# Kernel optimization log

Measured on AMD Instinct MI355X. Metric: run time of the kernel, lower is better.

The kernel has to match this reference:

```python
import jax, jax.numpy as jnp
import numpy as np

B, H, W0, C0 = 64, 50, 500, 3
TOPK = 10
OUT_SHAPE = (50, 3)


def _p(key, shape, scale=0.02):
    return (jax.random.normal(key, shape, dtype=jnp.float32) * scale)


def setup_inputs() -> dict:
    key = jax.random.key(0)
    ks = jax.random.split(key, 20)
    flat_dim = 128 * H * (W0 // 100) + TOPK * (32 + 64 + 128) * H  # 144000
    return {
        "x": jax.random.normal(ks[0], (B, H, W0, C0), dtype=jnp.float32),
        "c1w1": _p(ks[1], (C0, 32)), "c1b1": jnp.zeros((32,), jnp.float32),
        "c1w2": _p(ks[2], (32, 32)), "c1b2": jnp.zeros((32,), jnp.float32),
        "a1W": _p(ks[3], (H, 32)), "a1b": jnp.zeros((H, W0), jnp.float32),
        "c2w1": _p(ks[4], (32, 64)), "c2b1": jnp.zeros((64,), jnp.float32),
        "c2w2": _p(ks[5], (64, 64)), "c2b2": jnp.zeros((64,), jnp.float32),
        "a2W": _p(ks[6], (H, 64)), "a2b": jnp.zeros((H, W0 // 5), jnp.float32),
        "c3w1": _p(ks[7], (64, 128)), "c3b1": jnp.zeros((128,), jnp.float32),
        "c3w2": _p(ks[8], (128, 128)), "c3b2": jnp.zeros((128,), jnp.float32),
        "a3W": _p(ks[9], (H, 128)), "a3b": jnp.zeros((H, W0 // 25), jnp.float32),
        "fc1w": _p(ks[10], (flat_dim, 1024)), "fc1b": jnp.zeros((1024,), jnp.float32),
        "fc2w": _p(ks[11], (1024, 1024)), "fc2b": jnp.zeros((1024,), jnp.float32),
        "fc3w": _p(ks[12], (1024, OUT_SHAPE[0] * OUT_SHAPE[1])),
        "fc3b": jnp.zeros((OUT_SHAPE[0] * OUT_SHAPE[1],), jnp.float32),
    }


def _conv1x1_relu(x, w, b):
    # x: (B,H,W,Cin) channels-last; 1x1 conv == per-pixel matmul
    return jax.nn.relu(jnp.einsum('bhwc,co->bhwo', x, w) + b)


def _att_topk(x, Wm, bm, k):
    # x: (B,H,W,C); Wm: (H,C); bm: (H,W). Batched over all H rows at once.
    e = jnp.tanh(jnp.einsum('bhwc,hc->bhw', x, Wm) + bm[None])
    _, idx = jax.lax.top_k(e, k)                       # (B,H,k), sorted desc
    feats = jnp.take_along_axis(x, idx[..., None], axis=2)  # (B,H,k,C)
    return feats.reshape(x.shape[0], -1)  # row-major (h,k,c) matches torch cat


def _maxpool_w(x, p):
    b, h, w, c = x.shape
    return x.reshape(b, h, w // p, p, c).max(axis=3)


def reference(x, c1w1, c1b1, c1w2, c1b2, a1W, a1b, c2w1, c2b1, c2w2, c2b2,
              a2W, a2b, c3w1, c3b1, c3w2, c3b2, a3W, a3b,
              fc1w, fc1b, fc2w, fc2b, fc3w, fc3b):
    b = x.shape[0]
    x1 = _conv1x1_relu(_conv1x1_relu(x, c1w1, c1b1), c1w2, c1b2)   # (B,H,500,32)
    xa1 = _att_topk(x1, a1W, a1b, TOPK)
    x2 = _maxpool_w(x1, 5)                                          # (B,H,100,32)
    x2 = _conv1x1_relu(_conv1x1_relu(x2, c2w1, c2b1), c2w2, c2b2)   # (B,H,100,64)
    xa2 = _att_topk(x2, a2W, a2b, TOPK)
    x3 = _maxpool_w(x2, 5)                                          # (B,H,20,64)
    x3 = _conv1x1_relu(_conv1x1_relu(x3, c3w1, c3b1), c3w2, c3b2)   # (B,H,20,128)
    xa3 = _att_topk(x3, a3W, a3b, TOPK)
    xp = _maxpool_w(x3, 4)                                          # (B,H,5,128)
    # torch flattens NCHW: transpose to (B,C,H,W) before flatten
    xf = jnp.transpose(xp, (0, 3, 1, 2)).reshape(b, -1)
    z = jnp.concatenate([xa1, xa2, xa3, xf], axis=1)                # (B,144000)
    z = jax.nn.relu(z @ fc1w + fc1b)
    z = z @ fc2w + fc2b  # fc2 has no activation in the original
    # dropout is identity at inference
    z = z @ fc3w + fc3b
    return z.reshape(b, *OUT_SHAPE)
```

## Files before the change

kernel.cpp:

```cpp
#include <hip/hip_runtime.h>
#include <math.h>

#define DEV __device__ __forceinline__
DEV float frelu(float x) { return x > 0.f ? x : 0.f; }

typedef float f4 __attribute__((ext_vector_type(4)));
typedef short bf16x8 __attribute__((ext_vector_type(8)));
typedef int   i2x  __attribute__((ext_vector_type(2)));

DEV unsigned pack_hi2(float a, float b) {
    return (__float_as_uint(b) & 0xFFFF0000u) | (__float_as_uint(a) >> 16);
}
DEV float hi_part(float a) {
    return __uint_as_float(__float_as_uint(a) & 0xFFFF0000u);
}

#define DPP_ADD(v, ctrl) \
    ((v) + __int_as_float(__builtin_amdgcn_update_dpp(0, __float_as_int(v), (ctrl), 0xf, 0xf, true)))

DEV float rdlane(float v, int l) {
    return __int_as_float(__builtin_amdgcn_readlane(__float_as_int(v), l));
}

#define NG1 8
__global__ __launch_bounds__(256) void k_s1(
    const float* __restrict__ x,
    const float* __restrict__ w1, const float* __restrict__ b1,
    const float* __restrict__ w2, const float* __restrict__ b2,
    const float* __restrict__ aW, const float* __restrict__ ab,
    float* __restrict__ x1p, float* __restrict__ e1)
{
    __shared__ float v1s[4][2][32];
    int tid = threadIdx.x;
    int wv = tid >> 6, lane = tid & 63;
    int half = lane >> 5, o = lane & 31;
    int hs = blockIdx.x * 8 + wv * 2 + half;

    float W1c0 = w1[o], W1c1 = w1[32 + o], W1c2 = w1[64 + o], B1 = b1[o];
    float W2[32];
#pragma unroll
    for (int i = 0; i < 32; ++i) W2[i] = w2[i * 32 + o];
    float B2 = b2[o];
    float* vs = &v1s[wv][half][0];

#pragma unroll 1
    for (int i = 0; i < NG1; ++i) {
        int g = hs * NG1 + i;
        int b = g / 5000, r = g % 5000, h = r / 100, pw = r % 100;
        float AWo = aW[h * 32 + o];
        const float* xrow = x + (size_t)((b * 50 + h) * 500) * 3;
        float vmax = 0.f;
#pragma unroll 1
        for (int j = 0; j < 5; ++j) {
            int w = pw * 5 + j;
            float x0 = xrow[w * 3 + 0], x1v = xrow[w * 3 + 1], x2v = xrow[w * 3 + 2];
            float v1 = frelu(fmaf(x0, W1c0, fmaf(x1v, W1c1, fmaf(x2v, W1c2, B1))));
            vs[o] = v1;
            float a2 = B2;
#pragma unroll
            for (int q = 0; q < 32; q += 4) {
                float4 v4 = *(const float4*)&vs[q];
                a2 = fmaf(v4.x, W2[q + 0], a2);
                a2 = fmaf(v4.y, W2[q + 1], a2);
                a2 = fmaf(v4.z, W2[q + 2], a2);
                a2 = fmaf(v4.w, W2[q + 3], a2);
            }
            float t = frelu(a2);
            vmax = fmaxf(vmax, t);
            float ep = t * AWo;
            ep = DPP_ADD(ep, 0x111);
            ep = DPP_ADD(ep, 0x112);
            ep = DPP_ADD(ep, 0x114);
            ep = DPP_ADD(ep, 0x118);
            ep = DPP_ADD(ep, 0x142);
            if (o == 31) e1[(b * 50 + h) * 500 + w] = ep + ab[h * 500 + w];
        }
        x1p[(size_t)g * 32 + o] = vmax;
    }
}

#define NG2 16
__global__ __launch_bounds__(256) void k_s2(
    const float* __restrict__ x1p,
    const float* __restrict__ w1, const float* __restrict__ b1,
    const float* __restrict__ w2, const float* __restrict__ b2,
    const float* __restrict__ aW, const float* __restrict__ ab,
    float* __restrict__ x2p, float* __restrict__ e2)
{
    __shared__ float v1s[4][64];
    int tid = threadIdx.x;
    int wv = tid >> 6, o = tid & 63;
    int slot = blockIdx.x * 4 + wv;

    float W1[32];
#pragma unroll
    for (int i = 0; i < 32; ++i) W1[i] = w1[i * 64 + o];
    float W2[64];
#pragma unroll
    for (int i = 0; i < 64; ++i) W2[i] = w2[i * 64 + o];
    float B1 = b1[o], B2 = b2[o];
    float* vs = &v1s[wv][0];

#pragma unroll 1
    for (int i = 0; i < NG2; ++i) {
        int g = slot * NG2 + i;
        int b = g / 1000, r = g % 1000, h = r / 20, pw = r % 20;
        float AWo = aW[h * 64 + o];
        float vmax = 0.f;
#pragma unroll 1
        for (int j = 0; j < 5; ++j) {
            int w = pw * 5 + j;
            const float* in = x1p + (size_t)((b * 50 + h) * 100 + w) * 32;
            float a1 = B1;
#pragma unroll
            for (int q = 0; q < 32; q += 4) {
                float4 a4 = *(const float4*)&in[q];
                a1 = fmaf(a4.x, W1[q + 0], a1);
                a1 = fmaf(a4.y, W1[q + 1], a1);
                a1 = fmaf(a4.z, W1[q + 2], a1);
                a1 = fmaf(a4.w, W1[q + 3], a1);
            }
            vs[o] = frelu(a1);
            float a2 = B2;
#pragma unroll
            for (int q = 0; q < 64; q += 4) {
                float4 v4 = *(const float4*)&vs[q];
                a2 = fmaf(v4.x, W2[q + 0], a2);
                a2 = fmaf(v4.y, W2[q + 1], a2);
                a2 = fmaf(v4.z, W2[q + 2], a2);
                a2 = fmaf(v4.w, W2[q + 3], a2);
            }
            float t = frelu(a2);
            vmax = fmaxf(vmax, t);
            float ep = t * AWo;
            ep = DPP_ADD(ep, 0x111);
            ep = DPP_ADD(ep, 0x112);
            ep = DPP_ADD(ep, 0x114);
            ep = DPP_ADD(ep, 0x118);
            ep = DPP_ADD(ep, 0x142);
            ep = DPP_ADD(ep, 0x143);
            if (o == 63) e2[(b * 50 + h) * 100 + w] = ep + ab[h * 100 + w];
        }
        x2p[(size_t)g * 64 + o] = vmax;
    }
}

#define NG3 8
__global__ __launch_bounds__(256) void k_s3(
    const float* __restrict__ x2p,
    const float* __restrict__ w1, const float* __restrict__ b1,
    const float* __restrict__ w2, const float* __restrict__ b2,
    const float* __restrict__ aW, const float* __restrict__ ab,
    float* __restrict__ x3p, float* __restrict__ e3)
{
    __shared__ float v1s[2][128];
    __shared__ float epart[2][2];
    int tid = threadIdx.x;
    int wv = tid >> 6, lane = tid & 63;
    int slot = wv >> 1, oh = wv & 1;
    int o = oh * 64 + lane;
    int gs = blockIdx.x * 2 + slot;

    float W1[64];
#pragma unroll
    for (int i = 0; i < 64; ++i) W1[i] = w1[i * 128 + o];
    float W2[128];
#pragma unroll
    for (int i = 0; i < 128; ++i) W2[i] = w2[i * 128 + o];
    float B1 = b1[o], B2 = b2[o];

#pragma unroll 1
    for (int i = 0; i < NG3; ++i) {
        int g = gs * NG3 + i;
        int b = g / 250, r = g % 250, h = r / 5, pw = r % 5;
        float AWo = aW[h * 128 + o];
        float vmax = 0.f;
#pragma unroll 1
        for (int j = 0; j < 4; ++j) {
            int w = pw * 4 + j;
            const float* in = x2p + (size_t)((b * 50 + h) * 20 + w) * 64;
            float a1a = B1, a1b = 0.f;
#pragma unroll
            for (int q = 0; q < 64; q += 8) {
                float4 a4 = *(const float4*)&in[q];
                float4 b4 = *(const float4*)&in[q + 4];
                a1a = fmaf(a4.x, W1[q + 0], a1a);
                a1b = fmaf(a4.y, W1[q + 1], a1b);
                a1a = fmaf(a4.z, W1[q + 2], a1a);
                a1b = fmaf(a4.w, W1[q + 3], a1b);
                a1a = fmaf(b4.x, W1[q + 4], a1a);
                a1b = fmaf(b4.y, W1[q + 5], a1b);
                a1a = fmaf(b4.z, W1[q + 6], a1a);
                a1b = fmaf(b4.w, W1[q + 7], a1b);
            }
            v1s[slot][o] = frelu(a1a + a1b);
            __syncthreads();
            float a2a = B2, a2b = 0.f, a2c = 0.f, a2d = 0.f;
#pragma unroll
            for (int q = 0; q < 128; q += 8) {
                float4 a4 = *(const float4*)&v1s[slot][q];
                float4 b4 = *(const float4*)&v1s[slot][q + 4];
                a2a = fmaf(a4.x, W2[q + 0], a2a);
                a2b = fmaf(a4.y, W2[q + 1], a2b);
                a2c = fmaf(a4.z, W2[q + 2], a2c);
                a2d = fmaf(a4.w, W2[q + 3], a2d);
                a2a = fmaf(b4.x, W2[q + 4], a2a);
                a2b = fmaf(b4.y, W2[q + 5], a2b);
                a2c = fmaf(b4.z, W2[q + 6], a2c);
                a2d = fmaf(b4.w, W2[q + 7], a2d);
            }
            float t = frelu((a2a + a2b) + (a2c + a2d));
            vmax = fmaxf(vmax, t);
            float ep = t * AWo;
            ep = DPP_ADD(ep, 0x111);
            ep = DPP_ADD(ep, 0x112);
            ep = DPP_ADD(ep, 0x114);
            ep = DPP_ADD(ep, 0x118);
            ep = DPP_ADD(ep, 0x142);
            ep = DPP_ADD(ep, 0x143);
            if (lane == 63) epart[slot][oh] = ep;
            __syncthreads();
            if (lane == 63 && oh == 0)
                e3[(b * 50 + h) * 20 + w] = epart[slot][0] + epart[slot][1] + ab[h * 20 + w];
        }
        x3p[(size_t)g * 128 + o] = vmax;
    }
}

__global__ __launch_bounds__(64) void k_t1(
    const float* __restrict__ e1, const float* __restrict__ x,
    const float* __restrict__ w1, const float* __restrict__ b1,
    const float* __restrict__ w2, const float* __restrict__ b2,
    float* __restrict__ z)
{
    int blk = blockIdx.x; int b = blk / 50; int h = blk % 50;
    int lane = threadIdx.x;
    const float* er = e1 + (b * 50 + h) * 500;
    float ev0 = er[lane];
    float ev1 = er[64 + lane];
    float ev2 = er[128 + lane];
    float ev3 = er[192 + lane];
    float ev4 = er[256 + lane];
    float ev5 = er[320 + lane];
    float ev6 = er[384 + lane];
    float ev7 = (448 + lane < 500) ? er[448 + lane] : -1e30f;

    for (int k = 0; k < 10; ++k) {
        float bv = ev0; int bi = lane;
        if (ev1 > bv) { bv = ev1; bi = 64 + lane; }
        if (ev2 > bv) { bv = ev2; bi = 128 + lane; }
        if (ev3 > bv) { bv = ev3; bi = 192 + lane; }
        if (ev4 > bv) { bv = ev4; bi = 256 + lane; }
        if (ev5 > bv) { bv = ev5; bi = 320 + lane; }
        if (ev6 > bv) { bv = ev6; bi = 384 + lane; }
        if (ev7 > bv) { bv = ev7; bi = 448 + lane; }
#pragma unroll
        for (int d = 1; d < 64; d <<= 1) {
            float ov = __shfl_xor(bv, d, 64); int oi = __shfl_xor(bi, d, 64);
            if (ov > bv || (ov == bv && oi < bi)) { bv = ov; bi = oi; }
        }
        bool me = (bi & 63) == lane; int cs = bi >> 6;
        if (me && cs == 0) ev0 = -1e30f;
        if (me && cs == 1) ev1 = -1e30f;
        if (me && cs == 2) ev2 = -1e30f;
        if (me && cs == 3) ev3 = -1e30f;
        if (me && cs == 4) ev4 = -1e30f;
        if (me && cs == 5) ev5 = -1e30f;
        if (me && cs == 6) ev6 = -1e30f;
        if (me && cs == 7) ev7 = -1e30f;

        const float* px = x + (size_t)((b * 50 + h) * 500 + bi) * 3;
        float x0 = px[0], x1v = px[1], x2v = px[2];
        int o = lane & 31;
        float v1 = frelu(fmaf(x0, w1[o], fmaf(x1v, w1[32 + o], fmaf(x2v, w1[64 + o], b1[o]))));
        float v2 = b2[o];
#pragma unroll 8
        for (int i = 0; i < 32; ++i) v2 = fmaf(rdlane(v1, i), w2[i * 32 + o], v2);
        if (lane < 32) z[(size_t)b * 112000 + h * 320 + k * 32 + o] = frelu(v2);
    }
}

__global__ __launch_bounds__(64) void k_t2(
    const float* __restrict__ e2, const float* __restrict__ x1p,
    const float* __restrict__ w1, const float* __restrict__ b1,
    const float* __restrict__ w2, const float* __restrict__ b2,
    float* __restrict__ z)
{
    int blk = blockIdx.x; int b = blk / 50; int h = blk % 50;
    int lane = threadIdx.x;
    const float* er = e2 + (b * 50 + h) * 100;
    float ev0 = er[lane];
    float ev1 = (64 + lane < 100) ? er[64 + lane] : -1e30f;

    for (int k = 0; k < 10; ++k) {
        float bv = ev0; int bi = lane;
        if (ev1 > bv) { bv = ev1; bi = 64 + lane; }
#pragma unroll
        for (int d = 1; d < 64; d <<= 1) {
            float ov = __shfl_xor(bv, d, 64); int oi = __shfl_xor(bi, d, 64);
            if (ov > bv || (ov == bv && oi < bi)) { bv = ov; bi = oi; }
        }
        bool me = (bi & 63) == lane; int cs = bi >> 6;
        if (me && cs == 0) ev0 = -1e30f;
        if (me && cs == 1) ev1 = -1e30f;

        const float* in = x1p + (size_t)((b * 50 + h) * 100 + bi) * 32;
        float v1p0 = b1[lane], v1p1 = 0.f;
#pragma unroll 8
        for (int i = 0; i < 32; i += 2) {
            v1p0 = fmaf(in[i], w1[i * 64 + lane], v1p0);
            v1p1 = fmaf(in[i + 1], w1[(i + 1) * 64 + lane], v1p1);
        }
        float v1 = frelu(v1p0 + v1p1);
        float v2p0 = b2[lane], v2p1 = 0.f;
#pragma unroll 8
        for (int i = 0; i < 64; i += 2) {
            v2p0 = fmaf(rdlane(v1, i), w2[i * 64 + lane], v2p0);
            v2p1 = fmaf(rdlane(v1, i + 1), w2[(i + 1) * 64 + lane], v2p1);
        }
        z[(size_t)b * 112000 + 16000 + h * 640 + k * 64 + lane] = frelu(v2p0 + v2p1);
    }
}

__global__ __launch_bounds__(64) void k_t3(
    const float* __restrict__ e3, const float* __restrict__ x2p,
    const float* __restrict__ w1, const float* __restrict__ b1,
    const float* __restrict__ w2, const float* __restrict__ b2,
    float* __restrict__ z)
{
    int blk = blockIdx.x; int b = blk / 50; int h = blk % 50;
    int lane = threadIdx.x;
    const float* er = e3 + (b * 50 + h) * 20;
    float ev0 = (lane < 20) ? er[lane] : -1e30f;

    for (int k = 0; k < 10; ++k) {
        float bv = ev0; int bi = lane;
#pragma unroll
        for (int d = 1; d < 64; d <<= 1) {
            float ov = __shfl_xor(bv, d, 64); int oi = __shfl_xor(bi, d, 64);
            if (ov > bv || (ov == bv && oi < bi)) { bv = ov; bi = oi; }
        }
        if (bi == lane) ev0 = -1e30f;
        const float* in = x2p + (size_t)((b * 50 + h) * 20 + bi) * 64;
        float v1a0 = b1[lane], v1a1 = 0.f, v1b0 = b1[lane + 64], v1b1 = 0.f;
#pragma unroll 8
        for (int i = 0; i < 64; i += 2) {
            float a0 = in[i], a1 = in[i + 1];
            v1a0 = fmaf(a0, w1[i * 128 + lane], v1a0);
            v1b0 = fmaf(a0, w1[i * 128 + lane + 64], v1b0);
            v1a1 = fmaf(a1, w1[(i + 1) * 128 + lane], v1a1);
            v1b1 = fmaf(a1, w1[(i + 1) * 128 + lane + 64], v1b1);
        }
        float v1a = frelu(v1a0 + v1a1), v1b = frelu(v1b0 + v1b1);
        float v2a0 = b2[lane], v2a1 = 0.f, v2b0 = b2[lane + 64], v2b1 = 0.f;
#pragma unroll 8
        for (int i = 0; i < 64; i += 2) {
            float s0 = rdlane(v1a, i), s1 = rdlane(v1a, i + 1);
            v2a0 = fmaf(s0, w2[i * 128 + lane], v2a0);
            v2b0 = fmaf(s0, w2[i * 128 + lane + 64], v2b0);
            v2a1 = fmaf(s1, w2[(i + 1) * 128 + lane], v2a1);
            v2b1 = fmaf(s1, w2[(i + 1) * 128 + lane + 64], v2b1);
        }
#pragma unroll 8
        for (int i = 0; i < 64; i += 2) {
            float s0 = rdlane(v1b, i), s1 = rdlane(v1b, i + 1);
            v2a0 = fmaf(s0, w2[(i + 64) * 128 + lane], v2a0);
            v2b0 = fmaf(s0, w2[(i + 64) * 128 + lane + 64], v2b0);
            v2a1 = fmaf(s1, w2[(i + 65) * 128 + lane], v2a1);
            v2b1 = fmaf(s1, w2[(i + 65) * 128 + lane + 64], v2b1);
        }
        size_t base = (size_t)b * 112000 + 48000 + h * 1280 + k * 128;
        z[base + lane] = frelu(v2a0 + v2a1);
        z[base + lane + 64] = frelu(v2b0 + v2b1);
    }
}

__global__ __launch_bounds__(256) void k_zt(const float* __restrict__ z, float* __restrict__ zT)
{
    __shared__ float t[64][65];
    int f0 = blockIdx.x * 64;
    int tid = threadIdx.x;
    int fl = tid & 63, q = tid >> 6;
#pragma unroll
    for (int rr = 0; rr < 16; ++rr) {
        int m = q * 16 + rr;
        t[m][fl] = z[(size_t)m * 112000 + f0 + fl];
    }
    __syncthreads();
    int m2 = tid & 63;
#pragma unroll
    for (int rr = 0; rr < 16; ++rr) {
        int fl2 = q * 16 + rr;
        zT[(size_t)(f0 + fl2) * 64 + m2] = t[m2][fl2];
    }
}

__global__ __launch_bounds__(256) void k_xf(const float* __restrict__ x3p, float* __restrict__ zT)
{
    __shared__ float t[64][129];
    int blk = blockIdx.x;
    int h = blk / 5, pw = blk % 5;
    int tid = threadIdx.x;
    for (int idx = tid; idx < 64 * 128; idx += 256) {
        int m = idx >> 7, c = idx & 127;
        t[m][c] = x3p[(size_t)((m * 50 + h) * 5 + pw) * 128 + c];
    }
    __syncthreads();
    for (int idx = tid; idx < 64 * 128; idx += 256) {
        int c = idx >> 6, m = idx & 63;
        zT[(size_t)(112000 + c * 250 + h * 5 + pw) * 64 + m] = t[m][c];
    }
}

__global__ __launch_bounds__(256, 3) void k_gemm1(
    const float* __restrict__ AT, const float* __restrict__ W,
    float* __restrict__ part)
{
    __shared__ char smem[24576];
    const int t = threadIdx.x;
    const int lane = t & 63;
    const int wv = t >> 6;
    const int n0 = blockIdx.x << 7;
    const int kc = blockIdx.y;

    const int nw = t & 127, kqi = t >> 7;
    const int ma = t & 63,  kqa = t >> 6;

    int wadrW[4];
#pragma unroll
    for (int q = 0; q < 4; ++q)
        wadrW[q] = nw * 64 + (((kqi * 2 + (q >> 1)) ^ (nw & 3)) << 4) + ((q & 1) << 3);
    int wadrA[2];
#pragma unroll
    for (int q = 0; q < 2; ++q)
        wadrA[q] = 16384 + ma * 64 + ((kqa ^ (ma & 3)) << 4) + (q << 3);

    const int c = lane & 15, hi = lane >> 4;
    int rW[2], rA[4];
#pragma unroll
    for (int i = 0; i < 2; ++i) {
        int nl = (2 * wv + i) * 16 + c;
        rW[i] = nl * 64 + ((hi ^ (c & 3)) << 4);
    }
#pragma unroll
    for (int mf = 0; mf < 4; ++mf) {
        int ml = mf * 16 + c;
        rA[mf] = 16384 + ml * 64 + ((hi ^ (c & 3)) << 4);
    }

    f4 acc[2][4];
#pragma unroll
    for (int i = 0; i < 2; ++i)
#pragma unroll
        for (int mf = 0; mf < 4; ++mf) acc[i][mf] = (f4)0.f;

    const float* Wp = W + ((size_t)kc * 1152 + kqi * 16) * 1024 + (n0 + nw);
    const float* Ap = AT + ((size_t)kc * 1152 + kqa * 8) * 64 + ma;

    float gw[16], ga[8];
#pragma unroll
    for (int j = 0; j < 16; ++j) gw[j] = Wp[(size_t)j * 1024];
#pragma unroll
    for (int j = 0; j < 8; ++j) ga[j] = Ap[j * 64];
    Wp += 32768; Ap += 2048;

#pragma unroll 1
    for (int cc = 0; cc < 36; ++cc) {
        i2x whv[4], wlv[4], ahv[2], alv[2];
#pragma unroll
        for (int q = 0; q < 4; ++q) {
            float x0 = gw[q * 4 + 0], x1 = gw[q * 4 + 1];
            float x2 = gw[q * 4 + 2], x3 = gw[q * 4 + 3];
            whv[q].x = pack_hi2(x0, x1); whv[q].y = pack_hi2(x2, x3);
            float l0 = x0 - hi_part(x0), l1 = x1 - hi_part(x1);
            float l2 = x2 - hi_part(x2), l3 = x3 - hi_part(x3);
            wlv[q].x = pack_hi2(l0, l1); wlv[q].y = pack_hi2(l2, l3);
        }
#pragma unroll
        for (int q = 0; q < 2; ++q) {
            float x0 = ga[q * 4 + 0], x1 = ga[q * 4 + 1];
            float x2 = ga[q * 4 + 2], x3 = ga[q * 4 + 3];
            ahv[q].x = pack_hi2(x0, x1); ahv[q].y = pack_hi2(x2, x3);
            float l0 = x0 - hi_part(x0), l1 = x1 - hi_part(x1);
            float l2 = x2 - hi_part(x2), l3 = x3 - hi_part(x3);
            alv[q].x = pack_hi2(l0, l1); alv[q].y = pack_hi2(l2, l3);
        }
        __syncthreads();
#pragma unroll
        for (int q = 0; q < 4; ++q) {
            *(i2x*)(smem + wadrW[q]) = whv[q];
            *(i2x*)(smem + wadrW[q] + 8192) = wlv[q];
        }
#pragma unroll
        for (int q = 0; q < 2; ++q) {
            *(i2x*)(smem + wadrA[q]) = ahv[q];
            *(i2x*)(smem + wadrA[q] + 4096) = alv[q];
        }
        if (cc < 35) {
#pragma unroll
            for (int j = 0; j < 16; ++j) gw[j] = Wp[(size_t)j * 1024];
#pragma unroll
            for (int j = 0; j < 8; ++j) ga[j] = Ap[j * 64];
            Wp += 32768; Ap += 2048;
        }
        __syncthreads();

        bf16x8 fwh[2], fwl[2], fah[4], fal[4];
#pragma unroll
        for (int i = 0; i < 2; ++i) {
            fwh[i] = *(const bf16x8*)(smem + rW[i]);
            fwl[i] = *(const bf16x8*)(smem + rW[i] + 8192);
        }
#pragma unroll
        for (int mf = 0; mf < 4; ++mf) {
            fah[mf] = *(const bf16x8*)(smem + rA[mf]);
            fal[mf] = *(const bf16x8*)(smem + rA[mf] + 4096);
        }
#pragma unroll
        for (int i = 0; i < 2; ++i)
#pragma unroll
            for (int mf = 0; mf < 4; ++mf) {
                acc[i][mf] = __builtin_amdgcn_mfma_f32_16x16x32_bf16(fwh[i], fah[mf], acc[i][mf], 0, 0, 0);
                acc[i][mf] = __builtin_amdgcn_mfma_f32_16x16x32_bf16(fwh[i], fal[mf], acc[i][mf], 0, 0, 0);
                acc[i][mf] = __builtin_amdgcn_mfma_f32_16x16x32_bf16(fwl[i], fah[mf], acc[i][mf], 0, 0, 0);
            }
    }

    float* pb = part + ((size_t)kc * 1024 + n0) * 64;
#pragma unroll
    for (int i = 0; i < 2; ++i) {
        int nf = 2 * wv + i;
#pragma unroll
        for (int mf = 0; mf < 4; ++mf) {
#pragma unroll
            for (int q = 0; q < 4; ++q) {
                int n = nf * 16 + hi * 4 + q;
                int m = mf * 16 + c;
                pb[(size_t)n * 64 + m] = acc[i][mf][q];
            }
        }
    }
}

__global__ __launch_bounds__(256) void k_gemm(
    const float* __restrict__ AT, const float* __restrict__ W,
    float* __restrict__ part, int K, int N, int KC)
{
    int n = blockIdx.x * 256 + threadIdx.x;
    int kc = blockIdx.y;
    int k0 = kc * KC;
    int k1 = k0 + KC; if (k1 > K) k1 = K;
    float acc[64];
#pragma unroll
    for (int m = 0; m < 64; ++m) acc[m] = 0.f;
#pragma unroll 2
    for (int k = k0; k < k1; ++k) {
        float wv = W[(size_t)k * N + n];
        const float4* Ak4 = (const float4*)(AT + (size_t)k * 64);
#pragma unroll
        for (int mq = 0; mq < 16; ++mq) {
            float4 a = Ak4[mq];
            acc[4 * mq + 0] = fmaf(a.x, wv, acc[4 * mq + 0]);
            acc[4 * mq + 1] = fmaf(a.y, wv, acc[4 * mq + 1]);
            acc[4 * mq + 2] = fmaf(a.z, wv, acc[4 * mq + 2]);
            acc[4 * mq + 3] = fmaf(a.w, wv, acc[4 * mq + 3]);
        }
    }
    float4* p4 = (float4*)(part + ((size_t)kc * N + n) * 64);
#pragma unroll
    for (int mq = 0; mq < 16; ++mq)
        p4[mq] = make_float4(acc[4 * mq], acc[4 * mq + 1], acc[4 * mq + 2], acc[4 * mq + 3]);
}

__global__ __launch_bounds__(256) void k_redA(
    const float* __restrict__ part, float* __restrict__ pp)
{
    int id = blockIdx.x * 256 + threadIdx.x;
    int r = id & 16383; int s = id >> 14;
    const f4* p = (const f4*)part;
    f4 v = (f4)0.f;
#pragma unroll 5
    for (int cidx = s * 25; cidx < s * 25 + 25; ++cidx)
        v += p[(size_t)cidx * 16384 + r];
    ((f4*)pp)[(size_t)s * 16384 + r] = v;
}

__global__ __launch_bounds__(256) void k_redB(
    const float* __restrict__ pp, const float* __restrict__ bias,
    float* __restrict__ h1T)
{
    int id = blockIdx.x * 256 + threadIdx.x;
    int mq = id & 15, n = id >> 4;
    const f4* p = (const f4*)pp;
    f4 s = (f4)0.f;
#pragma unroll
    for (int cidx = 0; cidx < 5; ++cidx) s += p[(size_t)cidx * 16384 + id];
    float bv = bias[n];
    s += bv;
    s.x = frelu(s.x); s.y = frelu(s.y); s.z = frelu(s.z); s.w = frelu(s.w);
    *(f4*)(h1T + (size_t)n * 64 + mq * 4) = s;
}

__global__ __launch_bounds__(256) void k_red(
    const float* __restrict__ part, const float* __restrict__ bias,
    float* __restrict__ outM, int N, int C)
{
    int id = blockIdx.x * 256 + threadIdx.x;
    int mq = id & 15, n = id >> 4;
    f4 s = (f4)0.f;
    for (int cidx = 0; cidx < C; ++cidx)
        s += *(const f4*)(part + ((size_t)cidx * N + n) * 64 + mq * 4);
    float bv = bias[n];
    s += bv;
    outM[(size_t)(mq * 4 + 0) * N + n] = s.x;
    outM[(size_t)(mq * 4 + 1) * N + n] = s.y;
    outM[(size_t)(mq * 4 + 2) * N + n] = s.z;
    outM[(size_t)(mq * 4 + 3) * N + n] = s.w;
}

__global__ __launch_bounds__(192) void k_fc3(
    const float* __restrict__ h2M, const float* __restrict__ w3,
    const float* __restrict__ b3, float* __restrict__ out)
{
    int m = blockIdx.x;
    int o = threadIdx.x;
    int oc = o < 150 ? o : 149;
    const float* hr = h2M + (size_t)m * 1024;
    float s = b3[oc];
#pragma unroll 8
    for (int k = 0; k < 1024; ++k) s = fmaf(hr[k], w3[k * 150 + oc], s);
    if (o < 150) out[m * 150 + o] = s;
}

extern "C" void kernel_launch(void* const* d_in, const int* in_sizes, int n_in,
                              void* d_out, int out_size, void* d_ws, size_t ws_size,
                              hipStream_t stream) {
    const float* X    = (const float*)d_in[0];
    const float* c1w1 = (const float*)d_in[1];
    const float* c1b1 = (const float*)d_in[2];
    const float* c1w2 = (const float*)d_in[3];
    const float* c1b2 = (const float*)d_in[4];
    const float* a1W  = (const float*)d_in[5];
    const float* a1b  = (const float*)d_in[6];
    const float* c2w1 = (const float*)d_in[7];
    const float* c2b1 = (const float*)d_in[8];
    const float* c2w2 = (const float*)d_in[9];
    const float* c2b2 = (const float*)d_in[10];
    const float* a2W  = (const float*)d_in[11];
    const float* a2b  = (const float*)d_in[12];
    const float* c3w1 = (const float*)d_in[13];
    const float* c3b1 = (const float*)d_in[14];
    const float* c3w2 = (const float*)d_in[15];
    const float* c3b2 = (const float*)d_in[16];
    const float* a3W  = (const float*)d_in[17];
    const float* a3b  = (const float*)d_in[18];
    const float* fc1w = (const float*)d_in[19];
    const float* fc1b = (const float*)d_in[20];
    const float* fc2w = (const float*)d_in[21];
    const float* fc2b = (const float*)d_in[22];
    const float* fc3w = (const float*)d_in[23];
    const float* fc3b = (const float*)d_in[24];

    float* ws  = (float*)d_ws;
    float* x1p = ws;
    float* x2p = ws + 10240000;
    float* x3p = ws + 14336000;
    float* e1  = ws + 16384000;
    float* e2  = ws + 17984000;
    float* e3  = ws + 18304000;
    float* z   = ws + 18368000;
    float* zT  = ws + 25536000;
    float* p1  = ws;
    float* pp  = ws + 16384000;
    float* h1T = ws + 16600000;
    float* p2  = ws + 16700000;
    float* h2M = ws + 21000000;

    k_s1<<<5000, 256, 0, stream>>>(X, c1w1, c1b1, c1w2, c1b2, a1W, a1b, x1p, e1);
    k_t1<<<3200, 64, 0, stream>>>(e1, X, c1w1, c1b1, c1w2, c1b2, z);
    k_s2<<<1000, 256, 0, stream>>>(x1p, c2w1, c2b1, c2w2, c2b2, a2W, a2b, x2p, e2);
    k_t2<<<3200, 64, 0, stream>>>(e2, x1p, c2w1, c2b1, c2w2, c2b2, z);
    k_s3<<<1000, 256, 0, stream>>>(x2p, c3w1, c3b1, c3w2, c3b2, a3W, a3b, x3p, e3);
    k_t3<<<3200, 64, 0, stream>>>(e3, x2p, c3w1, c3b1, c3w2, c3b2, z);
    k_zt<<<1750, 256, 0, stream>>>(z, zT);
    k_xf<<<250, 256, 0, stream>>>(x3p, zT);

    k_gemm1<<<dim3(8, 125), 256, 0, stream>>>(zT, fc1w, p1);
    k_redA<<<320, 256, 0, stream>>>(p1, pp);
    k_redB<<<64, 256, 0, stream>>>(pp, fc1b, h1T);
    k_gemm<<<dim3(4, 64), 256, 0, stream>>>(h1T, fc2w, p2, 1024, 1024, 16);
    k_red<<<64, 256, 0, stream>>>(p2, fc2b, h2M, 1024, 64);
    k_fc3<<<64, 192, 0, stream>>>(h2M, fc3w, fc3b, (float*)d_out);
}
```

Measured before the change: 883.2 us.

## Replace LDS broadcast in conv second layers with DPP row-rotate cross-lane matvec

The second 1x1 conv layer in stages 1-3 used to write each lane's activation to shared memory and read it back as broadcast float4s. It now rotates values within 16-lane rows using DPP row_ror, plus xor shuffles across row groups, with the weights pre-permuted per lane to match the rotation order. Stage 3 keeps LDS only for the other wave's half. Stage 2 also halves the per-wave group count and doubles the grid for more parallelism. This trades LDS traffic for DPP and permute instructions and more weight registers, which could affect occupancy.

```diff
diff --git a/kernel.cpp b/kernel.cpp
--- a/kernel.cpp
+++ b/kernel.cpp
@@ -17,6 +17,11 @@
 
 #define DPP_ADD(v, ctrl) \
     ((v) + __int_as_float(__builtin_amdgcn_update_dpp(0, __float_as_int(v), (ctrl), 0xf, 0xf, true)))
+
+template<int CTRL>
+DEV float dppmov(float v) {
+    return __int_as_float(__builtin_amdgcn_update_dpp(0, __float_as_int(v), CTRL, 0xf, 0xf, true));
+}
 
 DEV float rdlane(float v, int l) {
     return __int_as_float(__builtin_amdgcn_readlane(__float_as_int(v), l));
@@ -30,18 +35,20 @@
     const float* __restrict__ aW, const float* __restrict__ ab,
     float* __restrict__ x1p, float* __restrict__ e1)
 {
-    __shared__ float v1s[4][2][32];
     int tid = threadIdx.x;
     int wv = tid >> 6, lane = tid & 63;
     int half = lane >> 5, o = lane & 31;
     int hs = blockIdx.x * 8 + wv * 2 + half;
 
     float W1c0 = w1[o], W1c1 = w1[32 + o], W1c2 = w1[64 + o], B1 = b1[o];
-    float W2[32];
-#pragma unroll
-    for (int i = 0; i < 32; ++i) W2[i] = w2[i * 32 + o];
+    float W2A[16], W2B[16];
+#pragma unroll
+    for (int s = 0; s < 16; ++s) {
+        int iA = ((((o & 15) + 16 - s) & 15) | (o & 16));
+        W2A[s] = w2[iA * 32 + o];
+        W2B[s] = w2[(iA ^ 16) * 32 + o];
+    }
     float B2 = b2[o];
-    float* vs = &v1s[wv][half][0];
 
 #pragma unroll 1
     for (int i = 0; i < NG1; ++i) {
@@ -55,17 +62,17 @@
             int w = pw * 5 + j;
             float x0 = xrow[w * 3 + 0], x1v = xrow[w * 3 + 1], x2v = xrow[w * 3 + 2];
             float v1 = frelu(fmaf(x0, W1c0, fmaf(x1v, W1c1, fmaf(x2v, W1c2, B1))));
-            vs[o] = v1;
-            float a2 = B2;
-#pragma unroll
-            for (int q = 0; q < 32; q += 4) {
-                float4 v4 = *(const float4*)&vs[q];
-                a2 = fmaf(v4.x, W2[q + 0], a2);
-                a2 = fmaf(v4.y, W2[q + 1], a2);
-                a2 = fmaf(v4.z, W2[q + 2], a2);
-                a2 = fmaf(v4.w, W2[q + 3], a2);
-            }
-            float t = frelu(a2);
+            float v1x = __shfl_xor(v1, 16, 64);
+            float aA = fmaf(v1, W2A[0], B2);
+            float aB = v1x * W2B[0];
+#define S1ROT(s) \
+            aA = fmaf(dppmov<0x120 + s>(v1),  W2A[s], aA); \
+            aB = fmaf(dppmov<0x120 + s>(v1x), W2B[s], aB);
+            S1ROT(1) S1ROT(2) S1ROT(3) S1ROT(4) S1ROT(5)
+            S1ROT(6) S1ROT(7) S1ROT(8) S1ROT(9) S1ROT(10)
+            S1ROT(11) S1ROT(12) S1ROT(13) S1ROT(14) S1ROT(15)
+#undef S1ROT
+            float t = frelu(aA + aB);
             vmax = fmaxf(vmax, t);
             float ep = t * AWo;
             ep = DPP_ADD(ep, 0x111);
@@ -79,7 +86,7 @@
     }
 }
 
-#define NG2 16
+#define NG2 8
 __global__ __launch_bounds__(256) void k_s2(
     const float* __restrict__ x1p,
     const float* __restrict__ w1, const float* __restrict__ b1,
@@ -87,7 +94,6 @@
     const float* __restrict__ aW, const float* __restrict__ ab,
     float* __restrict__ x2p, float* __restrict__ e2)
 {
-    __shared__ float v1s[4][64];
     int tid = threadIdx.x;
     int wv = tid >> 6, o = tid & 63;
     int slot = blockIdx.x * 4 + wv;
@@ -95,11 +101,15 @@
     float W1[32];
 #pragma unroll
     for (int i = 0; i < 32; ++i) W1[i] = w1[i * 64 + o];
-    float W2[64];
-#pragma unroll
-    for (int i = 0; i < 64; ++i) W2[i] = w2[i * 64 + o];
+    float W2r[4][16];
+#pragma unroll
+    for (int gg = 0; gg < 4; ++gg)
+#pragma unroll
+        for (int s = 0; s < 16; ++s) {
+            int idx = ((((o & 15) + 16 - s) & 15) | ((o & 48) ^ (gg << 4)));
+            W2r[gg][s] = w2[idx * 64 + o];
+        }
     float B1 = b1[o], B2 = b2[o];
-    float* vs = &v1s[wv][0];
 
 #pragma unroll 1
     for (int i = 0; i < NG2; ++i) {
@@ -120,17 +130,24 @@
                 a1 = fmaf(a4.z, W1[q + 2], a1);
                 a1 = fmaf(a4.w, W1[q + 3], a1);
             }
-            vs[o] = frelu(a1);
-            float a2 = B2;
-#pragma unroll
-            for (int q = 0; q < 64; q += 4) {
-                float4 v4 = *(const float4*)&vs[q];
-                a2 = fmaf(v4.x, W2[q + 0], a2);
-                a2 = fmaf(v4.y, W2[q + 1], a2);
-                a2 = fmaf(v4.z, W2[q + 2], a2);
-                a2 = fmaf(v4.w, W2[q + 3], a2);
-            }
-            float t = frelu(a2);
+            float v1r = frelu(a1);
+            float v16 = __shfl_xor(v1r, 16, 64);
+            float v32 = __shfl_xor(v1r, 32, 64);
+            float v48 = __shfl_xor(v1r, 48, 64);
+            float c0 = fmaf(v1r, W2r[0][0], B2);
+            float c1 = v16 * W2r[1][0];
+            float c2 = v32 * W2r[2][0];
+            float c3 = v48 * W2r[3][0];
+#define S2ROT(s) \
+            c0 = fmaf(dppmov<0x120 + s>(v1r), W2r[0][s], c0); \
+            c1 = fmaf(dppmov<0x120 + s>(v16), W2r[1][s], c1); \
+            c2 = fmaf(dppmov<0x120 + s>(v32), W2r[2][s], c2); \
+            c3 = fmaf(dppmov<0x120 + s>(v48), W2r[3][s], c3);
+            S2ROT(1) S2ROT(2) S2ROT(3) S2ROT(4) S2ROT(5)
+            S2ROT(6) S2ROT(7) S2ROT(8) S2ROT(9) S2ROT(10)
+            S2ROT(11) S2ROT(12) S2ROT(13) S2ROT(14) S2ROT(15)
+#undef S2ROT
+            float t = frelu((c0 + c1) + (c2 + c3));
             vmax = fmaxf(vmax, t);
             float ep = t * AWo;
             ep = DPP_ADD(ep, 0x111);
@@ -164,10 +181,19 @@
     float W1[64];
 #pragma unroll
     for (int i = 0; i < 64; ++i) W1[i] = w1[i * 128 + o];
-    float W2[128];
-#pragma unroll
-    for (int i = 0; i < 128; ++i) W2[i] = w2[i * 128 + o];
+    float W2o[4][16];
+#pragma unroll
+    for (int gg = 0; gg < 4; ++gg)
+#pragma unroll
+        for (int s = 0; s < 16; ++s) {
+            int idx = oh * 64 + ((((lane & 15) + 16 - s) & 15) | ((lane & 48) ^ (gg << 4)));
+            W2o[gg][s] = w2[idx * 128 + o];
+        }
+    float W2x[64];
+#pragma unroll
+    for (int i = 0; i < 64; ++i) W2x[i] = w2[((oh ^ 1) * 64 + i) * 128 + o];
     float B1 = b1[o], B2 = b2[o];
+    int xbase = (oh ^ 1) * 64;
 
 #pragma unroll 1
     for (int i = 0; i < NG3; ++i) {
@@ -193,23 +219,35 @@
                 a1a = fmaf(b4.z, W1[q + 6], a1a);
                 a1b = fmaf(b4.w, W1[q + 7], a1b);
             }
-            v1s[slot][o] = frelu(a1a + a1b);
+            float myv = frelu(a1a + a1b);
+            v1s[slot][o] = myv;
             __syncthreads();
-            float a2a = B2, a2b = 0.f, a2c = 0.f, a2d = 0.f;
-#pragma unroll
-            for (int q = 0; q < 128; q += 8) {
-                float4 a4 = *(const float4*)&v1s[slot][q];
-                float4 b4 = *(const float4*)&v1s[slot][q + 4];
-                a2a = fmaf(a4.x, W2[q + 0], a2a);
-                a2b = fmaf(a4.y, W2[q + 1], a2b);
-                a2c = fmaf(a4.z, W2[q + 2], a2c);
-                a2d = fmaf(a4.w, W2[q + 3], a2d);
-                a2a = fmaf(b4.x, W2[q + 4], a2a);
-                a2b = fmaf(b4.y, W2[q + 5], a2b);
-                a2c = fmaf(b4.z, W2[q + 6], a2c);
-                a2d = fmaf(b4.w, W2[q + 7], a2d);
+            float v16 = __shfl_xor(myv, 16, 64);
+            float v32 = __shfl_xor(myv, 32, 64);
+            float v48 = __shfl_xor(myv, 48, 64);
+            float c0 = fmaf(myv, W2o[0][0], B2);
+            float c1 = v16 * W2o[1][0];
+            float c2 = v32 * W2o[2][0];
+            float c3 = v48 * W2o[3][0];
+#define S3ROT(s) \
+            c0 = fmaf(dppmov<0x120 + s>(myv), W2o[0][s], c0); \
+            c1 = fmaf(dppmov<0x120 + s>(v16), W2o[1][s], c1); \
+            c2 = fmaf(dppmov<0x120 + s>(v32), W2o[2][s], c2); \
+            c3 = fmaf(dppmov<0x120 + s>(v48), W2o[3][s], c3);
+            S3ROT(1) S3ROT(2) S3ROT(3) S3ROT(4) S3ROT(5)
+            S3ROT(6) S3ROT(7) S3ROT(8) S3ROT(9) S3ROT(10)
+            S3ROT(11) S3ROT(12) S3ROT(13) S3ROT(14) S3ROT(15)
+#undef S3ROT
+            float d0 = 0.f, d1 = 0.f, d2 = 0.f, d3 = 0.f;
+#pragma unroll
+            for (int q = 0; q < 64; q += 4) {
+                float4 v4 = *(const float4*)&v1s[slot][xbase + q];
+                d0 = fmaf(v4.x, W2x[q + 0], d0);
+                d1 = fmaf(v4.y, W2x[q + 1], d1);
+                d2 = fmaf(v4.z, W2x[q + 2], d2);
+                d3 = fmaf(v4.w, W2x[q + 3], d3);
             }
-            float t = frelu((a2a + a2b) + (a2c + a2d));
+            float t = frelu(((c0 + c1) + (c2 + c3)) + ((d0 + d1) + (d2 + d3)));
             vmax = fmaxf(vmax, t);
             float ep = t * AWo;
             ep = DPP_ADD(ep, 0x111);
@@ -678,7 +716,7 @@
 
     k_s1<<<5000, 256, 0, stream>>>(X, c1w1, c1b1, c1w2, c1b2, a1W, a1b, x1p, e1);
     k_t1<<<3200, 64, 0, stream>>>(e1, X, c1w1, c1b1, c1w2, c1b2, z);
-    k_s2<<<1000, 256, 0, stream>>>(x1p, c2w1, c2b1, c2w2, c2b2, a2W, a2b, x2p, e2);
+    k_s2<<<2000, 256, 0, stream>>>(x1p, c2w1, c2b1, c2w2, c2b2, a2W, a2b, x2p, e2);
     k_t2<<<3200, 64, 0, stream>>>(e2, x1p, c2w1, c2b1, c2w2, c2b2, z);
     k_s3<<<1000, 256, 0, stream>>>(x2p, c3w1, c3b1, c3w2, c3b2, a3W, a3b, x3p, e3);
     k_t3<<<3200, 64, 0, stream>>>(e3, x2p, c3w1, c3b1, c3w2, c3b2, z);
```

Result: slower. 923.0 us (+4.5%).

## Compute stage-1 conv2 with bf16x3 MFMA, one block per image row

Applied to the files above, without the earlier changes.

Rewrites the first-stage kernel so each block handles one (batch, row) of 500 pixels, with four waves each taking a 125-pixel segment. The 32x32 second 1x1 conv now runs on 16x16x32 bf16 MFMA instructions, using a three-way bf16 split of weights and activations to keep near-fp32 accuracy. Results are staged in padded LDS tiles for the width-5 maxpool, and the attention score is reduced with cross-lane shuffles. The aim is to replace the scalar FMA loop and its per-pixel LDS broadcast with matrix-core work, at the cost of six MFMAs per fragment and some leftover rounding error from the split.

```diff
diff --git a/kernel.cpp b/kernel.cpp
--- a/kernel.cpp
+++ b/kernel.cpp
@@ -14,6 +14,14 @@
 DEV float hi_part(float a) {
     return __uint_as_float(__float_as_uint(a) & 0xFFFF0000u);
 }
+DEV bf16x8 pack8(const float* v) {
+    union { unsigned u[4]; bf16x8 b; } r;
+    r.u[0] = pack_hi2(v[0], v[1]);
+    r.u[1] = pack_hi2(v[2], v[3]);
+    r.u[2] = pack_hi2(v[4], v[5]);
+    r.u[3] = pack_hi2(v[6], v[7]);
+    return r.b;
+}
 
 #define DPP_ADD(v, ctrl) \
     ((v) + __int_as_float(__builtin_amdgcn_update_dpp(0, __float_as_int(v), (ctrl), 0xf, 0xf, true)))
@@ -22,7 +30,6 @@
     return __int_as_float(__builtin_amdgcn_readlane(__float_as_int(v), l));
 }
 
-#define NG1 8
 __global__ __launch_bounds__(256) void k_s1(
     const float* __restrict__ x,
     const float* __restrict__ w1, const float* __restrict__ b1,
@@ -30,53 +37,123 @@
     const float* __restrict__ aW, const float* __restrict__ ab,
     float* __restrict__ x1p, float* __restrict__ e1)
 {
-    __shared__ float v1s[4][2][32];
+    __shared__ float tl[4][80 * 33];
     int tid = threadIdx.x;
-    int wv = tid >> 6, lane = tid & 63;
-    int half = lane >> 5, o = lane & 31;
-    int hs = blockIdx.x * 8 + wv * 2 + half;
-
-    float W1c0 = w1[o], W1c1 = w1[32 + o], W1c2 = w1[64 + o], B1 = b1[o];
-    float W2[32];
-#pragma unroll
-    for (int i = 0; i < 32; ++i) W2[i] = w2[i * 32 + o];
-    float B2 = b2[o];
-    float* vs = &v1s[wv][half][0];
+    int seg = tid >> 6, lane = tid & 63;
+    int row = blockIdx.x;
+    int h = row % 50;
+    int c = lane & 15, hi = lane >> 4;
+
+    float W1r0[8], W1r1[8], W1r2[8], B1r[8];
+#pragma unroll
+    for (int j = 0; j < 8; ++j) {
+        int k = hi * 8 + j;
+        W1r0[j] = w1[k]; W1r1[j] = w1[32 + k]; W1r2[j] = w1[64 + k]; B1r[j] = b1[k];
+    }
+    bf16x8 Wh[2], Wm[2], Wl[2];
+#pragma unroll
+    for (int i = 0; i < 2; ++i) {
+        float vh[8], vm[8], vl[8];
+#pragma unroll
+        for (int j = 0; j < 8; ++j) {
+            float wv = w2[(hi * 8 + j) * 32 + i * 16 + c];
+            float hh = hi_part(wv); float r1 = wv - hh;
+            float mm = hi_part(r1);
+            vh[j] = hh; vm[j] = mm; vl[j] = r1 - mm;
+        }
+        Wh[i] = pack8(vh); Wm[i] = pack8(vm); Wl[i] = pack8(vl);
+    }
+    float aWr[2][4], b2r[2][4];
+#pragma unroll
+    for (int i = 0; i < 2; ++i)
+#pragma unroll
+        for (int q = 0; q < 4; ++q) {
+            int o = i * 16 + hi * 4 + q;
+            aWr[i][q] = aW[h * 32 + o];
+            b2r[i][q] = b2[o];
+        }
+
+    const float* xrow = x + (size_t)row * 1500;
+    float* tw = &tl[seg][0];
+
+#define S1_FRAG(fv, slot)                                                     \
+    {                                                                          \
+        int px = seg * 125 + (fv) * 16 + c;                                    \
+        int pxc = px < 500 ? px : 499;                                         \
+        float x0 = xrow[pxc * 3], x1v = xrow[pxc * 3 + 1], x2v = xrow[pxc * 3 + 2]; \
+        float vh[8], vm[8], vl[8];                                             \
+        _Pragma("unroll")                                                      \
+        for (int j = 0; j < 8; ++j) {                                          \
+            float v = frelu(fmaf(x0, W1r0[j], fmaf(x1v, W1r1[j], fmaf(x2v, W1r2[j], B1r[j])))); \
+            float hh = hi_part(v); float r1 = v - hh;                          \
+            float mm = hi_part(r1);                                            \
+            vh[j] = hh; vm[j] = mm; vl[j] = r1 - mm;                           \
+        }                                                                      \
+        bf16x8 Bh = pack8(vh), Bm = pack8(vm), Bl = pack8(vl);                 \
+        f4 a0 = (f4)0.f, a1 = (f4)0.f;                                         \
+        a0 = __builtin_amdgcn_mfma_f32_16x16x32_bf16(Wh[0], Bh, a0, 0, 0, 0);  \
+        a0 = __builtin_amdgcn_mfma_f32_16x16x32_bf16(Wh[0], Bm, a0, 0, 0, 0);  \
+        a0 = __builtin_amdgcn_mfma_f32_16x16x32_bf16(Wm[0], Bh, a0, 0, 0, 0);  \
+        a0 = __builtin_amdgcn_mfma_f32_16x16x32_bf16(Wh[0], Bl, a0, 0, 0, 0);  \
+        a0 = __builtin_amdgcn_mfma_f32_16x16x32_bf16(Wl[0], Bh, a0, 0, 0, 0);  \
+        a0 = __builtin_amdgcn_mfma_f32_16x16x32_bf16(Wm[0], Bm, a0, 0, 0, 0);  \
+        a1 = __builtin_amdgcn_mfma_f32_16x16x32_bf16(Wh[1], Bh, a1, 0, 0, 0);  \
+        a1 = __builtin_amdgcn_mfma_f32_16x16x32_bf16(Wh[1], Bm, a1, 0, 0, 0);  \
+        a1 = __builtin_amdgcn_mfma_f32_16x16x32_bf16(Wm[1], Bh, a1, 0, 0, 0);  \
+        a1 = __builtin_amdgcn_mfma_f32_16x16x32_bf16(Wh[1], Bl, a1, 0, 0, 0);  \
+        a1 = __builtin_amdgcn_mfma_f32_16x16x32_bf16(Wl[1], Bh, a1, 0, 0, 0);  \
+        a1 = __builtin_amdgcn_mfma_f32_16x16x32_bf16(Wm[1], Bm, a1, 0, 0, 0);  \
+        f4 t0, t1;                                                             \
+        _Pragma("unroll")                                                      \
+        for (int q = 0; q < 4; ++q) {                                          \
+            t0[q] = frelu(a0[q] + b2r[0][q]);                                  \
+            t1[q] = frelu(a1[q] + b2r[1][q]);                                  \
+        }                                                                      \
+        *(f4*)&tw[(slot) * 33 + hi * 4] = t0;                                  \
+        *(f4*)&tw[(slot) * 33 + 16 + hi * 4] = t1;                             \
+        float ep = t0[0] * aWr[0][0] + t0[1] * aWr[0][1]                       \
+                 + t0[2] * aWr[0][2] + t0[3] * aWr[0][3]                       \
+                 + t1[0] * aWr[1][0] + t1[1] * aWr[1][1]                       \
+                 + t1[2] * aWr[1][2] + t1[3] * aWr[1][3];                      \
+        ep += __shfl_xor(ep, 16, 64);                                          \
+        ep += __shfl_xor(ep, 32, 64);                                          \
+        if (lane < 16 && ((fv) < 7 || c < 13))                                 \
+            e1[(size_t)row * 500 + px] = ep + ab[h * 500 + px];                \
+    }
 
 #pragma unroll 1
-    for (int i = 0; i < NG1; ++i) {
-        int g = hs * NG1 + i;
-        int b = g / 5000, r = g % 5000, h = r / 100, pw = r % 100;
-        float AWo = aW[h * 32 + o];
-        const float* xrow = x + (size_t)((b * 50 + h) * 500) * 3;
-        float vmax = 0.f;
+    for (int f = 0; f < 5; ++f) S1_FRAG(f, f * 16 + c)
+#pragma unroll
+    for (int it = 0; it < 2; ++it) {
+        int u = lane + it * 64;
+        int g = u >> 3, qd = u & 7;
+        f4 mx = *(f4*)&tw[(g * 5 + 0) * 33 + qd * 4];
+#pragma unroll
+        for (int p = 1; p < 5; ++p) {
+            f4 v = *(f4*)&tw[(g * 5 + p) * 33 + qd * 4];
+            mx[0] = fmaxf(mx[0], v[0]); mx[1] = fmaxf(mx[1], v[1]);
+            mx[2] = fmaxf(mx[2], v[2]); mx[3] = fmaxf(mx[3], v[3]);
+        }
+        *(f4*)(x1p + ((size_t)row * 100 + seg * 25 + g) * 32 + qd * 4) = mx;
+    }
 #pragma unroll 1
-        for (int j = 0; j < 5; ++j) {
-            int w = pw * 5 + j;
-            float x0 = xrow[w * 3 + 0], x1v = xrow[w * 3 + 1], x2v = xrow[w * 3 + 2];
-            float v1 = frelu(fmaf(x0, W1c0, fmaf(x1v, W1c1, fmaf(x2v, W1c2, B1))));
-            vs[o] = v1;
-            float a2 = B2;
-#pragma unroll
-            for (int q = 0; q < 32; q += 4) {
-                float4 v4 = *(const float4*)&vs[q];
-                a2 = fmaf(v4.x, W2[q + 0], a2);
-                a2 = fmaf(v4.y, W2[q + 1], a2);
-                a2 = fmaf(v4.z, W2[q + 2], a2);
-                a2 = fmaf(v4.w, W2[q + 3], a2);
+    for (int f = 5; f < 8; ++f) S1_FRAG(f, (f - 5) * 16 + c)
+#pragma unroll
+    for (int it = 0; it < 2; ++it) {
+        int u = lane + it * 64;
+        if (u < 72) {
+            int g = u >> 3, qd = u & 7;
+            f4 mx = *(f4*)&tw[(g * 5 + 0) * 33 + qd * 4];
+#pragma unroll
+            for (int p = 1; p < 5; ++p) {
+                f4 v = *(f4*)&tw[(g * 5 + p) * 33 + qd * 4];
+                mx[0] = fmaxf(mx[0], v[0]); mx[1] = fmaxf(mx[1], v[1]);
+                mx[2] = fmaxf(mx[2], v[2]); mx[3] = fmaxf(mx[3], v[3]);
             }
-            float t = frelu(a2);
-            vmax = fmaxf(vmax, t);
-            float ep = t * AWo;
-            ep = DPP_ADD(ep, 0x111);
-            ep = DPP_ADD(ep, 0x112);
-            ep = DPP_ADD(ep, 0x114);
-            ep = DPP_ADD(ep, 0x118);
-            ep = DPP_ADD(ep, 0x142);
-            if (o == 31) e1[(b * 50 + h) * 500 + w] = ep + ab[h * 500 + w];
-        }
-        x1p[(size_t)g * 32 + o] = vmax;
-    }
+            *(f4*)(x1p + ((size_t)row * 100 + seg * 25 + 16 + g) * 32 + qd * 4) = mx;
+        }
+    }
+#undef S1_FRAG
 }
 
 #define NG2 16
@@ -676,7 +753,7 @@
     float* p2  = ws + 16700000;
     float* h2M = ws + 21000000;
 
-    k_s1<<<5000, 256, 0, stream>>>(X, c1w1, c1b1, c1w2, c1b2, a1W, a1b, x1p, e1);
+    k_s1<<<3200, 256, 0, stream>>>(X, c1w1, c1b1, c1w2, c1b2, a1W, a1b, x1p, e1);
     k_t1<<<3200, 64, 0, stream>>>(e1, X, c1w1, c1b1, c1w2, c1b2, z);
     k_s2<<<1000, 256, 0, stream>>>(x1p, c2w1, c2b1, c2w2, c2b2, a2W, a2b, x2p, e2);
     k_t2<<<3200, 64, 0, stream>>>(e2, x1p, c2w1, c2b1, c2w2, c2b2, z);
```

New measurement: 839.4 us. 1.05x faster.
